# Optimization experiments

Hardware: AMD Instinct MI355X
Metric: run time of the kernel (lower is better)

The kernel has to match this reference:

```python
import jax, jax.numpy as jnp
import numpy as np

B, T, C, H = 2, 2048, 1024, 16
D = C // H  # head_dim = 64


def setup_inputs() -> dict:
    key = jax.random.key(0)
    k1, k2, k3 = jax.random.split(key, 3)
    x = jax.random.normal(k1, (B, T, C), dtype=jnp.float32)
    Wqkv = jax.random.normal(k2, (C, 3 * C), dtype=jnp.float32) * (1.0 / np.sqrt(C))
    Wo = jax.random.normal(k3, (C, C), dtype=jnp.float32) * (1.0 / np.sqrt(C))
    bo = jnp.zeros((C,), dtype=jnp.float32)
    return {"x": x, "Wqkv": Wqkv, "Wo": Wo, "bo": bo}


def reference(x, Wqkv, Wo, bo):
    Bc, Tc, Cc = x.shape
    qkv = x @ Wqkv                                  # [B,T,3C]
    q, k, v = jnp.split(qkv, 3, axis=-1)
    # [B,T,C] -> [B,H,T,D]
    q = q.reshape(Bc, Tc, H, D).transpose(0, 2, 1, 3)
    k = k.reshape(Bc, Tc, H, D).transpose(0, 2, 1, 3)
    v = v.reshape(Bc, Tc, H, D).transpose(0, 2, 1, 3)
    scale = 1.0 / np.sqrt(D)
    att = jnp.einsum('bhqd,bhkd->bhqk', q, k) * scale   # [B,H,T,T]
    causal = jnp.tril(jnp.ones((Tc, Tc), dtype=bool))
    att = jnp.where(causal[None, None], att, -jnp.inf)
    att = jax.nn.softmax(att, axis=-1)
    # dropout treated as identity (eval mode)
    y = jnp.einsum('bhqk,bhkd->bhqd', att, v)           # [B,H,T,D]
    y = y.transpose(0, 2, 1, 3).reshape(Bc, Tc, Cc)     # [B,T,C]
    return y @ Wo + bo
```

## Files before the change

### kernel.cpp

```cpp
#include <hip/hip_runtime.h>
#include <hip/hip_bf16.h>
#include <math.h>


typedef __attribute__((ext_vector_type(8))) short bf16x8;
typedef __attribute__((ext_vector_type(4))) float f32x4;

__device__ __forceinline__ float b2f(unsigned short u) {
    union { unsigned int i; float f; } x; x.i = ((unsigned int)u) << 16; return x.f;
}
__device__ __forceinline__ unsigned short f2b(float f) {
    __hip_bfloat16 h = __float2bfloat16(f);
    return *reinterpret_cast<unsigned short*>(&h);
}
__device__ __forceinline__ unsigned short f2b_rz(float f) {
    union { float f; unsigned int i; } u; u.f = f; return (unsigned short)(u.i >> 16);
}
__device__ __forceinline__ float fexp2(float x) {
#if __has_builtin(__builtin_amdgcn_exp2f)
    return __builtin_amdgcn_exp2f(x);
#else
    return exp2f(x);
#endif
}
__device__ __forceinline__ void gload_lds16(const void* g, void* l) {
    __builtin_amdgcn_global_load_lds(
        (__attribute__((address_space(1))) void*)g,
        (__attribute__((address_space(3))) void*)l, 16, 0, 0);
}

__device__ __forceinline__ void transpose_job64(
        const void* __restrict__ in, unsigned short* __restrict__ out,
        int Cc, int use_bf, int nscale, float scale,
        int c0, int r0, int tid, unsigned short (*t)[65]) {
    const unsigned short* inb = (const unsigned short*)in;
    const float* inf = (const float*)in;
    const int x = tid & 63, y = tid >> 6;
    #pragma unroll
    for (int i = 0; i < 64; i += 4) {
        size_t idx = (size_t)(r0 + y + i) * Cc + c0 + x;
        float v = use_bf ? b2f(inb[idx]) : inf[idx];
        if (c0 + x < nscale) v *= scale;
        t[y + i][x] = f2b(v);
    }
    __syncthreads();
    #pragma unroll
    for (int i = 0; i < 64; i += 4)
        out[(size_t)(c0 + y + i) * 1024 + r0 + x] = t[x][y + i];
}

__global__ __launch_bounds__(256) void prep_kernel(
        const void* __restrict__ xin, const void* __restrict__ Wqkv,
        const void* __restrict__ Wo, const void* __restrict__ bias,
        unsigned short* __restrict__ xb, unsigned short* __restrict__ WqkvT,
        unsigned short* __restrict__ WoT, unsigned short* __restrict__ bob,
        int* __restrict__ flag, float qscale) {
    __shared__ __align__(16) unsigned short t[64][65];
    __shared__ int det;
    const int tid = threadIdx.x, blk = blockIdx.x;

    if (tid < 64) {
        const unsigned short* xu = (const unsigned short*)xin;
        int cnt = 0;
        for (int i = tid; i < 1024; i += 64) {
            unsigned short u = xu[2 * i];
            int e = (u >> 7) & 0xFF;
            if (!((e == 0) || (e >= 96 && e <= 159))) cnt++;
        }
        #pragma unroll
        for (int m = 1; m < 64; m <<= 1) cnt += __shfl_xor(cnt, m);
        if (tid == 0) det = (cnt > 200) ? 0 : 1;
    }
    __syncthreads();
    const int use_bf = det;

    if (blk < 1024) {
        int base = blk * 4096;
        #pragma unroll
        for (int i = 0; i < 4; i++) {
            int i4 = base + (tid + 256 * i) * 4;
            if (use_bf) {
                *(ushort4*)(xb + i4) = *(const ushort4*)((const unsigned short*)xin + i4);
            } else {
                float4 f = *(const float4*)((const float*)xin + i4);
                ushort4 o;
                o.x = f2b(f.x); o.y = f2b(f.y); o.z = f2b(f.z); o.w = f2b(f.w);
                *(ushort4*)(xb + i4) = o;
            }
        }
    } else if (blk < 1792) {
        int tt = blk - 1024;
        int c0 = (tt % 48) * 64, r0 = (tt / 48) * 64;
        transpose_job64(Wqkv, WqkvT, 3072, use_bf, 1024, qscale, c0, r0, tid, t);
    } else if (blk < 2048) {
        int tt = blk - 1792;
        int c0 = (tt & 15) * 64, r0 = (tt >> 4) * 64;
        transpose_job64(Wo, WoT, 1024, use_bf, 0, 1.0f, c0, r0, tid, t);
    } else {
        int i4 = tid * 4;
        if (use_bf) {
            *(ushort4*)(bob + i4) = *(const ushort4*)((const unsigned short*)bias + i4);
        } else {
            float4 f = *(const float4*)((const float*)bias + i4);
            ushort4 o;
            o.x = f2b(f.x); o.y = f2b(f.y); o.z = f2b(f.z); o.w = f2b(f.w);
            *(ushort4*)(bob + i4) = o;
        }
        if (tid == 0) *flag = use_bf;
    }
}

__global__ __launch_bounds__(256, 2) void gemm_qkv(
        const unsigned short* __restrict__ A, const unsigned short* __restrict__ Bt,
        unsigned short* __restrict__ qb, unsigned short* __restrict__ kb,
        unsigned short* __restrict__ vt) {
    __shared__ __align__(16) unsigned short lA[128 * 64];
    __shared__ __align__(16) unsigned short lB[192 * 64];
    const int tid  = threadIdx.x;
    const int wave = tid >> 6, lane = tid & 63;
    const int g = lane >> 4, c = lane & 15;
    const int m0 = blockIdx.y * 128, n0 = blockIdx.x * 192;
    const int wr = (wave >> 1) * 64;
    const int wc = (wave & 1) * 96;
    const int srow = lane >> 3;
    const int sc8  = ((lane & 7) ^ ((lane >> 3) & 7)) * 8;

    f32x4 acc[4][6] = {};

    for (int k0 = 0; k0 < 1024; k0 += 64) {
        #pragma unroll
        for (int i = 0; i < 4; i++) {
            int seg = wave * 4 + i;
            int row = seg * 8 + srow;
            gload_lds16(A  + (size_t)(m0 + row) * 1024 + k0 + sc8, lA + seg * 512);
        }
        #pragma unroll
        for (int i = 0; i < 6; i++) {
            int seg = wave * 6 + i;
            int row = seg * 8 + srow;
            gload_lds16(Bt + (size_t)(n0 + row) * 1024 + k0 + sc8, lB + seg * 512);
        }
        __syncthreads();

        #pragma unroll
        for (int dk = 0; dk < 2; dk++) {
            const int off = ((4 * dk + g) ^ (c & 7)) << 3;
            bf16x8 af[4], bfv[6];
            #pragma unroll
            for (int i = 0; i < 4; i++)
                af[i]  = *(const bf16x8*)(lA + (wr + 16 * i + c) * 64 + off);
            #pragma unroll
            for (int i = 0; i < 6; i++)
                bfv[i] = *(const bf16x8*)(lB + (wc + 16 * i + c) * 64 + off);
            #pragma unroll
            for (int mi = 0; mi < 4; mi++)
                #pragma unroll
                for (int ni = 0; ni < 6; ni++)
                    acc[mi][ni] = __builtin_amdgcn_mfma_f32_16x16x32_bf16(
                        af[mi], bfv[ni], acc[mi][ni], 0, 0, 0);
        }
        __syncthreads();
    }

    const int bb  = m0 >> 11;
    const int kvb = (m0 & 2047) + wr;
    #pragma unroll
    for (int ni = 0; ni < 6; ni++) {
        const int colbase = n0 + wc + 16 * ni;
        if (colbase < 2048) {
            unsigned short* dst = (colbase < 1024) ? qb : kb;
            const int cb = (colbase & 1023) + c;
            #pragma unroll
            for (int mi = 0; mi < 4; mi++)
                #pragma unroll
                for (int r = 0; r < 4; r++) {
                    int row = m0 + wr + 16 * mi + 4 * g + r;
                    dst[(size_t)row * 1024 + cb] = f2b(acc[mi][ni][r]);
                }
        } else {
            const int cc2 = colbase - 2048;
            const int hb  = cc2 >> 6;
            const int d   = (cc2 & 63) + c;
            const int bh  = bb * 16 + hb;
            #pragma unroll
            for (int mi = 0; mi < 4; mi++) {
                int kv = kvb + 16 * mi + 4 * g;
                ushort4 pk;
                pk.x = f2b(acc[mi][ni][0]); pk.y = f2b(acc[mi][ni][1]);
                pk.z = f2b(acc[mi][ni][2]); pk.w = f2b(acc[mi][ni][3]);
                *(ushort4*)(vt + ((size_t)bh * 64 + d) * 2048 + kv) = pk;
            }
        }
    }
}

__global__ __launch_bounds__(256) void gemm_nt(
        const unsigned short* __restrict__ A, const unsigned short* __restrict__ Bt,
        void* __restrict__ C, const unsigned short* __restrict__ bias,
        const int* __restrict__ out_f32_flag, int M, int N, int K) {
    __shared__ __align__(16) unsigned short lA[128 * 64];
    __shared__ __align__(16) unsigned short lB[64 * 64];
    const int tid  = threadIdx.x;
    const int wave = tid >> 6, lane = tid & 63;
    const int g = lane >> 4, c = lane & 15;
    const int m0 = blockIdx.y * 128, n0 = blockIdx.x * 64;
    const int wm = wave * 32;
    const int srow = lane >> 3;
    const int sc8  = ((lane & 7) ^ ((lane >> 3) & 7)) * 8;

    f32x4 acc[2][4] = {};

    for (int k0 = 0; k0 < K; k0 += 64) {
        #pragma unroll
        for (int i = 0; i < 4; i++) {
            int seg = wave * 4 + i;
            int row = seg * 8 + srow;
            gload_lds16(A + (size_t)(m0 + row) * K + k0 + sc8, lA + seg * 512);
        }
        #pragma unroll
        for (int i = 0; i < 2; i++) {
            int seg = wave * 2 + i;
            int row = seg * 8 + srow;
            gload_lds16(Bt + (size_t)(n0 + row) * K + k0 + sc8, lB + seg * 512);
        }
        __syncthreads();

        #pragma unroll
        for (int dk = 0; dk < 2; dk++) {
            const int off = ((4 * dk + g) ^ (c & 7)) << 3;
            bf16x8 af[2], bfv[4];
            #pragma unroll
            for (int i = 0; i < 2; i++)
                af[i]  = *(const bf16x8*)(lA + (wm + 16 * i + c) * 64 + off);
            #pragma unroll
            for (int i = 0; i < 4; i++)
                bfv[i] = *(const bf16x8*)(lB + (16 * i + c) * 64 + off);
            #pragma unroll
            for (int mi = 0; mi < 2; mi++)
                #pragma unroll
                for (int ni = 0; ni < 4; ni++)
                    acc[mi][ni] = __builtin_amdgcn_mfma_f32_16x16x32_bf16(
                        af[mi], bfv[ni], acc[mi][ni], 0, 0, 0);
        }
        __syncthreads();
    }

    const bool f32out = out_f32_flag && (*out_f32_flag == 0);
    #pragma unroll
    for (int mi = 0; mi < 2; mi++)
        #pragma unroll
        for (int ni = 0; ni < 4; ni++)
            #pragma unroll
            for (int r = 0; r < 4; r++) {
                int row = m0 + wm + 16 * mi + 4 * g + r;
                int col = n0 + 16 * ni + c;
                float v = acc[mi][ni][r];
                if (bias) v += b2f(bias[col]);
                if (f32out) ((float*)C)[(size_t)row * N + col] = v;
                else ((unsigned short*)C)[(size_t)row * N + col] = f2b(v);
            }
}

template<bool MASKED>
__device__ __forceinline__ void tile_compute(
        const unsigned short* __restrict__ lKs, const unsigned short* __restrict__ lVts,
        unsigned short* __restrict__ P, const bf16x8* qB, f32x4* o,
        float& l_run, int wave, int lane, int g, int c) {
    const f32x4 sinit = {-12.f, -12.f, -12.f, -12.f};
    f32x4 s[4] = {sinit, sinit, sinit, sinit};
    #pragma unroll
    for (int nt = 0; nt < 4; nt++)
        #pragma unroll
        for (int dk = 0; dk < 2; dk++) {
            bf16x8 kA = *(const bf16x8*)(lKs + (16 * nt + c) * 64 + (((4 * dk + g) ^ (c & 7)) << 3));
            s[nt] = __builtin_amdgcn_mfma_f32_16x16x32_bf16(kA, qB[dk], s[nt], 0, 0, 0);
        }

    float rsum = 0.f;
    #pragma unroll
    for (int nt = 0; nt < 4; nt++) {
        unsigned long long pk = 0;
        #pragma unroll
        for (int r = 0; r < 4; r++) {
            float v = s[nt][r];
            if (MASKED) v = (16 * nt + 4 * g + r <= 16 * wave + c) ? v : -1e30f;
            float p = fexp2(v);
            rsum += p;
            pk |= ((unsigned long long)f2b_rz(p)) << (16 * r);
        }
        int kvl = 16 * nt + 4 * g;
        *(unsigned long long*)(P + c * 64 + (((kvl >> 3) ^ (c & 7)) << 3) + (kvl & 7)) = pk;
    }
    rsum += __shfl_xor(rsum, 16);
    rsum += __shfl_xor(rsum, 32);
    l_run += rsum;

    __asm__ volatile("s_waitcnt lgkmcnt(0)" ::: "memory");

    bf16x8 pf[2];
    #pragma unroll
    for (int kk = 0; kk < 2; kk++)
        pf[kk] = *(const bf16x8*)(P + c * 64 + (((4 * kk + g) ^ (c & 7)) << 3));
    #pragma unroll
    for (int ni = 0; ni < 4; ni++)
        #pragma unroll
        for (int kk = 0; kk < 2; kk++) {
            bf16x8 vf = *(const bf16x8*)(lVts + (16 * ni + c) * 64 + (((4 * kk + g) ^ (c & 7)) << 3));
            o[ni] = __builtin_amdgcn_mfma_f32_16x16x32_bf16(pf[kk], vf, o[ni], 0, 0, 0);
        }
    __asm__ volatile("" ::: "memory");
}

__global__ __launch_bounds__(256) void attn_kernel(
        const unsigned short* __restrict__ qb, const unsigned short* __restrict__ kb,
        const unsigned short* __restrict__ vt, unsigned short* __restrict__ Y) {
    __shared__ __align__(16) unsigned short lK[2][4096];
    __shared__ __align__(16) unsigned short lVt[2][4096];
    __shared__ __align__(16) unsigned short Pbuf[4][1024];

    const int tid = threadIdx.x, wave = tid >> 6, lane = tid & 63;
    const int g = lane >> 4, c = lane & 15;
    unsigned short* P = Pbuf[wave];
    const int srow = lane >> 3;
    const int sc8  = ((lane & 7) ^ ((lane >> 3) & 7)) * 8;

    const int rr = blockIdx.x >> 8, cc = blockIdx.x & 255;
    const int kslot = cc >> 3;
    const int j  = (rr & 1) ? kslot : (31 - kslot);
    const int bh = rr * 8 + (cc & 7);
    const int q0 = j * 64;
    const int b = bh >> 4, h = bh & 15;
    const int rbase = q0 + 16 * wave;

    const unsigned short* Qb  = qb + (size_t)b * 2048 * 1024 + h * 64;
    const unsigned short* Kb  = kb + (size_t)b * 2048 * 1024 + h * 64;
    const unsigned short* Vtb = vt + (size_t)bh * 64 * 2048;

    bf16x8 qB[2];
    #pragma unroll
    for (int dk = 0; dk < 2; dk++)
        qB[dk] = *(const bf16x8*)(Qb + (size_t)(rbase + c) * 1024 + 32 * dk + 8 * g);

    f32x4 o[4] = {};
    float l_run = 0.f;

    #pragma unroll 1
    for (int kv0 = 0; kv0 <= q0; kv0 += 128) {
        const bool do1 = (kv0 + 64 <= q0);
        #pragma unroll
        for (int i = 0; i < 2; i++) {
            int seg = wave * 2 + i;
            int row = seg * 8 + srow;
            gload_lds16(Kb  + (size_t)(kv0 + row) * 1024 + sc8, lK[0] + seg * 512);
            gload_lds16(Vtb + (size_t)row * 2048 + kv0 + sc8,   lVt[0] + seg * 512);
            if (do1) {
                gload_lds16(Kb  + (size_t)(kv0 + 64 + row) * 1024 + sc8, lK[1] + seg * 512);
                gload_lds16(Vtb + (size_t)row * 2048 + kv0 + 64 + sc8,   lVt[1] + seg * 512);
            }
        }
        __syncthreads();

        if (kv0 == q0)
            tile_compute<true >(lK[0], lVt[0], P, qB, o, l_run, wave, lane, g, c);
        else
            tile_compute<false>(lK[0], lVt[0], P, qB, o, l_run, wave, lane, g, c);
        if (do1) {
            if (kv0 + 64 == q0)
                tile_compute<true >(lK[1], lVt[1], P, qB, o, l_run, wave, lane, g, c);
            else
                tile_compute<false>(lK[1], lVt[1], P, qB, o, l_run, wave, lane, g, c);
        }
        __syncthreads();
    }

    float inv = 1.f / l_run;
    float il[4];
    #pragma unroll
    for (int r = 0; r < 4; r++)
        il[r] = __shfl(inv, (lane & 48) | (4 * g + r));
    #pragma unroll
    for (int ni = 0; ni < 4; ni++)
        #pragma unroll
        for (int r = 0; r < 4; r++) {
            int row = rbase + 4 * g + r;
            Y[(size_t)(b * 2048 + row) * 1024 + h * 64 + 16 * ni + c] =
                f2b(o[ni][r] * il[r]);
        }
}

extern "C" void kernel_launch(void* const* d_in, const int* in_sizes, int n_in,
                              void* d_out, int out_size, void* d_ws, size_t ws_size,
                              hipStream_t stream) {
    char* ws = (char*)d_ws;
    unsigned short* qb    = (unsigned short*)(ws);
    unsigned short* kb    = (unsigned short*)(ws + 8388608);
    unsigned short* vt    = (unsigned short*)(ws + 16777216);
    unsigned short* Y     = (unsigned short*)(ws + 25165824);
    unsigned short* WqkvT = (unsigned short*)(ws + 33554432);
    unsigned short* WoT   = (unsigned short*)(ws + 39845888);
    unsigned short* xb    = (unsigned short*)(ws + 41943040);
    unsigned short* bob   = (unsigned short*)(ws + 50331648);
    int*            flag  = (int*)(ws + 50333696);

    prep_kernel<<<2049, 256, 0, stream>>>(
        d_in[0], d_in[1], d_in[2], d_in[3], xb, WqkvT, WoT, bob, flag,
        0.125f * 1.4426950408889634f);

    gemm_qkv<<<dim3(16, 32), 256, 0, stream>>>(xb, WqkvT, qb, kb, vt);

    attn_kernel<<<1024, 256, 0, stream>>>(qb, kb, vt, Y);

    gemm_nt<<<dim3(16, 32), 256, 0, stream>>>(Y, WoT, d_out, bob, flag, 4096, 1024, 1024);
}
```

Baseline: 173.9 us.

## Load K and V fragments directly from global memory instead of staging in LDS

The attention kernel stops staging K and V^T tiles in shared memory through async global-to-LDS loads and block barriers. Each wave now loads its own MFMA operand fragments straight from global memory, with one 64-wide KV tile per iteration. It also adds s_setprio around the MFMA bursts and an occupancy hint in launch_bounds. This removes the __syncthreads barriers and LDS traffic. The cost is that all four waves redundantly fetch the same K/V data through L1/L2 with strided 16-byte loads, and there is no explicit prefetch to hide latency.

```diff
diff --git a/kernel.cpp b/kernel.cpp
--- a/kernel.cpp
+++ b/kernel.cpp
@@ -262,19 +262,35 @@
 }
 
 template<bool MASKED>
-__device__ __forceinline__ void tile_compute(
-        const unsigned short* __restrict__ lKs, const unsigned short* __restrict__ lVts,
+__device__ __forceinline__ void tile_direct(
+        const unsigned short* __restrict__ Kt,
+        const unsigned short* __restrict__ Vv,
         unsigned short* __restrict__ P, const bf16x8* qB, f32x4* o,
         float& l_run, int wave, int lane, int g, int c) {
     const f32x4 sinit = {-12.f, -12.f, -12.f, -12.f};
     f32x4 s[4] = {sinit, sinit, sinit, sinit};
+
+    bf16x8 kA[4][2];
     #pragma unroll
     for (int nt = 0; nt < 4; nt++)
         #pragma unroll
-        for (int dk = 0; dk < 2; dk++) {
-            bf16x8 kA = *(const bf16x8*)(lKs + (16 * nt + c) * 64 + (((4 * dk + g) ^ (c & 7)) << 3));
-            s[nt] = __builtin_amdgcn_mfma_f32_16x16x32_bf16(kA, qB[dk], s[nt], 0, 0, 0);
-        }
+        for (int dk = 0; dk < 2; dk++)
+            kA[nt][dk] = *(const bf16x8*)(Kt + (size_t)(16 * nt + c) * 1024 + 32 * dk + 8 * g);
+
+    __builtin_amdgcn_s_setprio(1);
+    #pragma unroll
+    for (int nt = 0; nt < 4; nt++)
+        #pragma unroll
+        for (int dk = 0; dk < 2; dk++)
+            s[nt] = __builtin_amdgcn_mfma_f32_16x16x32_bf16(kA[nt][dk], qB[dk], s[nt], 0, 0, 0);
+    __builtin_amdgcn_s_setprio(0);
+
+    bf16x8 vf[4][2];
+    #pragma unroll
+    for (int ni = 0; ni < 4; ni++)
+        #pragma unroll
+        for (int kk = 0; kk < 2; kk++)
+            vf[ni][kk] = *(const bf16x8*)(Vv + (size_t)(16 * ni + c) * 2048 + 32 * kk + 8 * g);
 
     float rsum = 0.f;
     #pragma unroll
@@ -301,28 +317,25 @@
     #pragma unroll
     for (int kk = 0; kk < 2; kk++)
         pf[kk] = *(const bf16x8*)(P + c * 64 + (((4 * kk + g) ^ (c & 7)) << 3));
+
+    __builtin_amdgcn_s_setprio(1);
     #pragma unroll
     for (int ni = 0; ni < 4; ni++)
         #pragma unroll
-        for (int kk = 0; kk < 2; kk++) {
-            bf16x8 vf = *(const bf16x8*)(lVts + (16 * ni + c) * 64 + (((4 * kk + g) ^ (c & 7)) << 3));
-            o[ni] = __builtin_amdgcn_mfma_f32_16x16x32_bf16(pf[kk], vf, o[ni], 0, 0, 0);
-        }
+        for (int kk = 0; kk < 2; kk++)
+            o[ni] = __builtin_amdgcn_mfma_f32_16x16x32_bf16(pf[kk], vf[ni][kk], o[ni], 0, 0, 0);
+    __builtin_amdgcn_s_setprio(0);
     __asm__ volatile("" ::: "memory");
 }
 
-__global__ __launch_bounds__(256) void attn_kernel(
+__global__ __launch_bounds__(256, 4) void attn_kernel(
         const unsigned short* __restrict__ qb, const unsigned short* __restrict__ kb,
         const unsigned short* __restrict__ vt, unsigned short* __restrict__ Y) {
-    __shared__ __align__(16) unsigned short lK[2][4096];
-    __shared__ __align__(16) unsigned short lVt[2][4096];
     __shared__ __align__(16) unsigned short Pbuf[4][1024];
 
     const int tid = threadIdx.x, wave = tid >> 6, lane = tid & 63;
     const int g = lane >> 4, c = lane & 15;
     unsigned short* P = Pbuf[wave];
-    const int srow = lane >> 3;
-    const int sc8  = ((lane & 7) ^ ((lane >> 3) & 7)) * 8;
 
     const int rr = blockIdx.x >> 8, cc = blockIdx.x & 255;
     const int kslot = cc >> 3;
@@ -345,32 +358,13 @@
     float l_run = 0.f;
 
     #pragma unroll 1
-    for (int kv0 = 0; kv0 <= q0; kv0 += 128) {
-        const bool do1 = (kv0 + 64 <= q0);
-        #pragma unroll
-        for (int i = 0; i < 2; i++) {
-            int seg = wave * 2 + i;
-            int row = seg * 8 + srow;
-            gload_lds16(Kb  + (size_t)(kv0 + row) * 1024 + sc8, lK[0] + seg * 512);
-            gload_lds16(Vtb + (size_t)row * 2048 + kv0 + sc8,   lVt[0] + seg * 512);
-            if (do1) {
-                gload_lds16(Kb  + (size_t)(kv0 + 64 + row) * 1024 + sc8, lK[1] + seg * 512);
-                gload_lds16(Vtb + (size_t)row * 2048 + kv0 + 64 + sc8,   lVt[1] + seg * 512);
-            }
-        }
-        __syncthreads();
-
+    for (int kv0 = 0; kv0 <= q0; kv0 += 64) {
+        const unsigned short* Kt = Kb + (size_t)kv0 * 1024;
+        const unsigned short* Vv = Vtb + kv0;
         if (kv0 == q0)
-            tile_compute<true >(lK[0], lVt[0], P, qB, o, l_run, wave, lane, g, c);
+            tile_direct<true >(Kt, Vv, P, qB, o, l_run, wave, lane, g, c);
         else
-            tile_compute<false>(lK[0], lVt[0], P, qB, o, l_run, wave, lane, g, c);
-        if (do1) {
-            if (kv0 + 64 == q0)
-                tile_compute<true >(lK[1], lVt[1], P, qB, o, l_run, wave, lane, g, c);
-            else
-                tile_compute<false>(lK[1], lVt[1], P, qB, o, l_run, wave, lane, g, c);
-        }
-        __syncthreads();
+            tile_direct<false>(Kt, Vv, P, qB, o, l_run, wave, lane, g, c);
     }
 
     float inv = 1.f / l_run;
```

New measurement: 256.8 us. 1.48x slower.

## Double-buffer K/V tiles to overlap loads with attention compute

Applied to the files above, without the earlier changes.

Replaces the load-two-tiles-then-compute loop with a software-pipelined double buffer: the next 64-key K/Vt tile is prefetched into the alternate LDS buffer while the current tile is computed, with a single barrier per tile. The diagonal tile is handled after the loop with the masked variant. It also adds a minimum-occupancy hint of 4 blocks per CU to launch_bounds, which may constrain register allocation. The goal is to hide global-to-LDS latency instead of stalling on it each iteration.

```diff
diff --git a/kernel.cpp b/kernel.cpp
--- a/kernel.cpp
+++ b/kernel.cpp
@@ -311,7 +311,7 @@
     __asm__ volatile("" ::: "memory");
 }
 
-__global__ __launch_bounds__(256) void attn_kernel(
+__global__ __launch_bounds__(256, 4) void attn_kernel(
         const unsigned short* __restrict__ qb, const unsigned short* __restrict__ kb,
         const unsigned short* __restrict__ vt, unsigned short* __restrict__ Y) {
     __shared__ __align__(16) unsigned short lK[2][4096];
@@ -344,34 +344,31 @@
     f32x4 o[4] = {};
     float l_run = 0.f;
 
+    #define STAGE_ATTN(T, BUF)                                                     \
+        {                                                                          \
+            int kvs = (T) * 64;                                                    \
+            _Pragma("unroll")                                                      \
+            for (int i = 0; i < 2; i++) {                                          \
+                int seg = wave * 2 + i;                                            \
+                int row = seg * 8 + srow;                                          \
+                gload_lds16(Kb  + (size_t)(kvs + row) * 1024 + sc8, lK[BUF] + seg * 512);  \
+                gload_lds16(Vtb + (size_t)row * 2048 + kvs + sc8,   lVt[BUF] + seg * 512); \
+            }                                                                      \
+        }
+
+    STAGE_ATTN(0, 0);
+    __syncthreads();
+    int cur = 0;
+
     #pragma unroll 1
-    for (int kv0 = 0; kv0 <= q0; kv0 += 128) {
-        const bool do1 = (kv0 + 64 <= q0);
-        #pragma unroll
-        for (int i = 0; i < 2; i++) {
-            int seg = wave * 2 + i;
-            int row = seg * 8 + srow;
-            gload_lds16(Kb  + (size_t)(kv0 + row) * 1024 + sc8, lK[0] + seg * 512);
-            gload_lds16(Vtb + (size_t)row * 2048 + kv0 + sc8,   lVt[0] + seg * 512);
-            if (do1) {
-                gload_lds16(Kb  + (size_t)(kv0 + 64 + row) * 1024 + sc8, lK[1] + seg * 512);
-                gload_lds16(Vtb + (size_t)row * 2048 + kv0 + 64 + sc8,   lVt[1] + seg * 512);
-            }
-        }
+    for (int t = 0; t < j; t++) {
+        STAGE_ATTN(t + 1, cur ^ 1);
+        tile_compute<false>(lK[cur], lVt[cur], P, qB, o, l_run, wave, lane, g, c);
         __syncthreads();
-
-        if (kv0 == q0)
-            tile_compute<true >(lK[0], lVt[0], P, qB, o, l_run, wave, lane, g, c);
-        else
-            tile_compute<false>(lK[0], lVt[0], P, qB, o, l_run, wave, lane, g, c);
-        if (do1) {
-            if (kv0 + 64 == q0)
-                tile_compute<true >(lK[1], lVt[1], P, qB, o, l_run, wave, lane, g, c);
-            else
-                tile_compute<false>(lK[1], lVt[1], P, qB, o, l_run, wave, lane, g, c);
-        }
-        __syncthreads();
-    }
+        cur ^= 1;
+    }
+    tile_compute<true>(lK[cur], lVt[cur], P, qB, o, l_run, wave, lane, g, c);
+    #undef STAGE_ATTN
 
     float inv = 1.f / l_run;
     float il[4];
```

After: 175.8 us. No clear change (+1.1%).
